# Kernel optimization log

Measured on AMD Instinct MI355X. Metric: run time of the kernel, lower is better.

## Reference

```python
import jax, jax.numpy as jnp
import numpy as np

N = 50000
E = 800000
IN_C = 128
HID = 256
OUT_C = 40


def setup_inputs() -> dict:
    key = jax.random.key(0)
    ks = jax.random.split(key, 12)
    def glorot(k, shape):
        lim = float(np.sqrt(6.0 / (shape[0] + shape[1])))
        return jax.random.uniform(k, shape, jnp.float32, -lim, lim)
    x = jax.random.normal(ks[0], (N, IN_C), jnp.float32)
    edge_index = jax.random.randint(ks[1], (2, E), 0, N, jnp.int64)
    edge_weight = jax.random.uniform(ks[2], (E,), jnp.float32)
    return {
        "x": x,
        "edge_index": edge_index,
        "edge_weight": edge_weight,
        "w1_rel": glorot(ks[3], (IN_C, HID)),
        "b1": jnp.zeros((HID,), jnp.float32),
        "w1_root": glorot(ks[4], (IN_C, HID)),
        "w2_rel": glorot(ks[5], (HID, HID)),
        "b2": jnp.zeros((HID,), jnp.float32),
        "w2_root": glorot(ks[6], (HID, HID)),
        "w_lin": glorot(ks[7], (2 * HID, OUT_C)),
        "b_lin": jnp.zeros((OUT_C,), jnp.float32),
    }


def graph_conv(x, src, dst, w, w_rel, b_rel, w_root):
    # PyG GraphConv (aggr='add'): lin_rel(scatter_add(x[src]*w)) + lin_root(x)
    msg = x[src] * w[:, None]                      # [E, F]
    agg = jax.ops.segment_sum(msg, dst, num_segments=N)  # [N, F]
    return agg @ w_rel + b_rel + x @ w_root


def reference(x, edge_index, edge_weight, w1_rel, b1, w1_root,
              w2_rel, b2, w2_root, w_lin, b_lin):
    src, dst = edge_index[0], edge_index[1]
    x1 = jax.nn.relu(graph_conv(x, src, dst, edge_weight, w1_rel, b1, w1_root))
    # dropout is a no-op in eval mode
    x2 = jax.nn.relu(graph_conv(x1, src, dst, edge_weight, w2_rel, b2, w2_root))
    h = jnp.concatenate([x1, x2], axis=-1)         # [N, 2*HID]
    logits = h @ w_lin + b_lin                     # [N, OUT_C]
    return jax.nn.log_softmax(logits, axis=-1)
```

## Files before the change

### kernel.cpp

```cpp
#include <hip/hip_runtime.h>
#include <hip/hip_bf16.h>
#include <hip/hip_fp16.h>
#include <math.h>


typedef __attribute__((ext_vector_type(8))) short short8;
typedef __attribute__((ext_vector_type(4))) float f32x4;

static __device__ __forceinline__ float bf2f(unsigned short u) {
    return __uint_as_float(((unsigned)u) << 16);
}

static __device__ __forceinline__ void fp8x4_to_f32(unsigned u, float* o) {
#if __has_builtin(__builtin_amdgcn_cvt_pk_f32_fp8)
    auto lo = __builtin_amdgcn_cvt_pk_f32_fp8((int)u, false);
    auto hi = __builtin_amdgcn_cvt_pk_f32_fp8((int)u, true);
    o[0] = lo[0]; o[1] = lo[1]; o[2] = hi[0]; o[3] = hi[1];
#else
#pragma unroll
    for (int i = 0; i < 4; ++i) {
        unsigned b = (u >> (8 * i)) & 0xffu;
        unsigned short hb = (unsigned short)(((b & 0x80u) << 8) | ((b & 0x7fu) << 7));
        o[i] = __half2float(__ushort_as_half(hb)) * 256.0f;
    }
#endif
}

static __device__ __forceinline__ unsigned f32_to_fp8(float f) {
    __half h = __float2half(f * 0.00390625f);
    unsigned short hb = __half_as_ushort(h);
    unsigned mag = hb & 0x7fffu;
    unsigned s = (hb >> 8) & 0x80u;
    unsigned v = (mag + 0x3fu + ((mag >> 7) & 1u)) >> 7;
    if (v > 0x7eu) v = 0x7eu;
    return s | v;
}

#define BH_EPB 16

__global__ __launch_bounds__(256) void prep_all(
    const int* __restrict__ ei, int E, int hist_blocks,
    int* __restrict__ bh_part,
    const float* __restrict__ x, __hip_bfloat16* __restrict__ xb,
    unsigned char* __restrict__ xb8, int NX8,
    const float* __restrict__ w1_rel, const float* __restrict__ w1_root,
    const float* __restrict__ w2_rel, const float* __restrict__ w2_root,
    const float* __restrict__ w_lin,
    __hip_bfloat16* __restrict__ w1relT, __hip_bfloat16* __restrict__ w1rootT,
    __hip_bfloat16* __restrict__ w2relT, __hip_bfloat16* __restrict__ w2rootT,
    __hip_bfloat16* __restrict__ wlinT)
{
    __shared__ int lh[256];
    const int t = threadIdx.x;
    if (blockIdx.x < (unsigned)hist_blocks) {
        lh[t] = 0;
        __syncthreads();
        const int base = blockIdx.x * (256 * BH_EPB);
#pragma unroll
        for (int i = 0; i < BH_EPB; ++i) {
            int e = base + i * 256 + t;
            if (e < E) atomicAdd(&lh[ei[E + e] >> 8], 1);
        }
        __syncthreads();
        bh_part[blockIdx.x * 256 + t] = lh[t];
        return;
    }
    int idx = (blockIdx.x - hist_blocks) * 256 + t;
    if (idx < NX8) {
        float4 a = *(const float4*)&x[(size_t)idx * 8];
        float4 b = *(const float4*)&x[(size_t)idx * 8 + 4];
        float f[8] = { a.x, a.y, a.z, a.w, b.x, b.y, b.z, b.w };
        __hip_bfloat16 o[8];
#pragma unroll
        for (int i = 0; i < 8; ++i) o[i] = __float2bfloat16(f[i]);
        *(short8*)&xb[(size_t)idx * 8] = *(short8*)o;
        unsigned p0 = 0, p1 = 0;
#pragma unroll
        for (int i = 0; i < 4; ++i) p0 |= f32_to_fp8(f[i]) << (8 * i);
#pragma unroll
        for (int i = 0; i < 4; ++i) p1 |= f32_to_fp8(f[4 + i]) << (8 * i);
        *(uint2*)&xb8[(size_t)idx * 8] = make_uint2(p0, p1);
        return;
    }
    idx -= NX8;
    if (idx < 65536) {
        const float* src = (idx < 32768) ? w1_rel : w1_root;
        __hip_bfloat16* dst = (idx < 32768) ? w1relT : w1rootT;
        int i = idx & 32767;
        int k = i >> 8, c = i & 255;
        dst[c * 128 + k] = __float2bfloat16(src[i]);
    } else if (idx < 196608) {
        int j = idx - 65536;
        const float* src = (j < 65536) ? w2_rel : w2_root;
        __hip_bfloat16* dst = (j < 65536) ? w2relT : w2rootT;
        int i = j & 65535;
        int k = i >> 8, c = i & 255;
        dst[c * 256 + k] = __float2bfloat16(src[i]);
    } else if (idx < 229376) {
        int i = idx - 196608;
        int seg = i >> 14, c = (i >> 8) & 63, k = i & 255;
        float v = (c < 40) ? w_lin[(size_t)(seg * 256 + k) * 40 + c] : 0.f;
        wlinT[i] = __float2bfloat16(v);
    }
}

__global__ __launch_bounds__(256) void scan_bsum(
    const int* __restrict__ bh_part, int hist_blocks,
    int* __restrict__ bpre, int* __restrict__ bend,
    int* __restrict__ bucket_cursor)
{
    __shared__ int sh[256];
    const int t = threadIdx.x;
    int a0 = 0, a1 = 0, a2 = 0, a3 = 0, a4 = 0, a5 = 0, a6 = 0, a7 = 0;
    int b = 0;
    for (; b + 8 <= hist_blocks; b += 8) {
        a0 += bh_part[(b + 0) * 256 + t];
        a1 += bh_part[(b + 1) * 256 + t];
        a2 += bh_part[(b + 2) * 256 + t];
        a3 += bh_part[(b + 3) * 256 + t];
        a4 += bh_part[(b + 4) * 256 + t];
        a5 += bh_part[(b + 5) * 256 + t];
        a6 += bh_part[(b + 6) * 256 + t];
        a7 += bh_part[(b + 7) * 256 + t];
    }
    for (; b < hist_blocks; ++b) a0 += bh_part[b * 256 + t];
    int v = ((a0 + a1) + (a2 + a3)) + ((a4 + a5) + (a6 + a7));
    sh[t] = v;
    __syncthreads();
#pragma unroll
    for (int off = 1; off < 256; off <<= 1) {
        int u = (t >= off) ? sh[t - off] : 0;
        __syncthreads();
        sh[t] += u;
        __syncthreads();
    }
    bpre[t]          = sh[t] - v;
    bend[t]          = sh[t];
    bucket_cursor[t] = sh[t] - v;
}

#define P1_EPB 8
__global__ __launch_bounds__(256) void part_kernel(
    const int* __restrict__ ei, const float* __restrict__ ew,
    int* __restrict__ bucket_cursor, uint2* __restrict__ part, int E)
{
    __shared__ int lhist[256];
    __shared__ int gbase[256];
    const int t = threadIdx.x;
    const int base = blockIdx.x * (256 * P1_EPB);
    lhist[t] = 0;
    __syncthreads();

    int pk[P1_EPB];
#pragma unroll
    for (int i = 0; i < P1_EPB; ++i) {
        int e = base + i * 256 + t;
        if (e < E) {
            int b = ei[E + e] >> 8;
            int r = atomicAdd(&lhist[b], 1);
            pk[i] = (b << 16) | r;
        } else pk[i] = -1;
    }
    __syncthreads();
    if (lhist[t] > 0) gbase[t] = atomicAdd(&bucket_cursor[t], lhist[t]);
    __syncthreads();
#pragma unroll
    for (int i = 0; i < P1_EPB; ++i) {
        if (pk[i] >= 0) {
            int e = base + i * 256 + t;
            int d = ei[E + e];
            unsigned short w16 = __half_as_ushort(__float2half(ew[e]));
            unsigned rec = ((unsigned)w16 << 16) | (unsigned)ei[e];
            int pos = gbase[pk[i] >> 16] + (pk[i] & 0xffff);
            part[pos] = make_uint2(rec, (unsigned)d);
        }
    }
}

__global__ __launch_bounds__(256) void fill2_kernel(
    const uint2* __restrict__ part, const int* __restrict__ bpre,
    const int* __restrict__ bend, int* __restrict__ row_ptr,
    unsigned* __restrict__ edges, int n)
{
    __shared__ int lcnt[256];
    __shared__ int excl[256];
    __shared__ int curs[256];
    const int b = blockIdx.x;
    const int t = threadIdx.x;
    const int node0 = b << 8;
    lcnt[t] = 0;
    __syncthreads();
    const int beg = bpre[b];
    const int end = bend[b];
    for (int i = beg + t; i < end; i += 256)
        atomicAdd(&lcnt[part[i].y & 255u], 1);
    __syncthreads();
    int v = lcnt[t];
    excl[t] = v;
    __syncthreads();
#pragma unroll
    for (int off = 1; off < 256; off <<= 1) {
        int u = (t >= off) ? excl[t - off] : 0;
        __syncthreads();
        excl[t] += u;
        __syncthreads();
    }
    const int base_t = beg + excl[t] - v;
    const int nd = node0 + t;
    if (nd <= n) row_ptr[nd] = base_t;
    curs[t] = base_t;
    __syncthreads();
    for (int i = beg + t; i < end; i += 256) {
        uint2 p = part[i];
        int slot = atomicAdd(&curs[p.y & 255u], 1);
        edges[slot] = p.x;
    }
}

template <int C>
__global__ __launch_bounds__(256) void gather_fp8(
    const unsigned char* __restrict__ feat8,
    const unsigned* __restrict__ edges,
    const int*  __restrict__ rp,
    __hip_bfloat16* __restrict__ agg, int n)
{
    const int node = (blockIdx.x * 256 + threadIdx.x) >> 6;
    const int lane = threadIdx.x & 63;
    if (node >= n) return;
    const int beg = __builtin_amdgcn_readfirstlane(rp[node]);
    const int end = __builtin_amdgcn_readfirstlane(rp[node + 1]);

    constexpr int EPW = (C == 128) ? 8 : 4;
    constexpr int LPR = 64 / EPW;
    const int es = lane / LPR;
    const int ch = lane % LPR;
    const unsigned coff = (unsigned)ch * 16;

    float acc[16] = {};

    auto accum16 = [&](uint4 u, float w) {
        unsigned uu[4] = { u.x, u.y, u.z, u.w };
#pragma unroll
        for (int q = 0; q < 4; ++q) {
            float f[4];
            fp8x4_to_f32(uu[q], f);
#pragma unroll
            for (int i = 0; i < 4; ++i)
                acc[q * 4 + i] = fmaf(f[i], w, acc[q * 4 + i]);
        }
    };

    auto unpack_w = [](unsigned p) {
        return __half2float(__ushort_as_half((unsigned short)(p >> 16)));
    };

    for (int base = beg; base < end; base += 64) {
        const int m = min(64, end - base);
        unsigned ev = edges[base + ((lane < m) ? lane : (m - 1))];
        if (lane >= m) ev &= 0xffffu;

        int s = 0;
        for (; s + 2 * EPW <= m; s += 2 * EPW) {
            int j0 = s + es, j1 = j0 + EPW;
            unsigned p0 = (unsigned)__shfl((int)ev, j0, 64);
            unsigned p1 = (unsigned)__shfl((int)ev, j1, 64);
            uint4 u0 = *(const uint4*)(feat8 + (size_t)(p0 & 0xffffu) * C + coff);
            uint4 u1 = *(const uint4*)(feat8 + (size_t)(p1 & 0xffffu) * C + coff);
            accum16(u0, unpack_w(p0));
            accum16(u1, unpack_w(p1));
        }
        for (; s < m; s += EPW) {
            int j = min(s + es, 63);
            unsigned p = (unsigned)__shfl((int)ev, j, 64);
            uint4 u = *(const uint4*)(feat8 + (size_t)(p & 0xffffu) * C + coff);
            accum16(u, unpack_w(p));
        }
    }

#pragma unroll
    for (int k = 0; k < 16; ++k) {
        if constexpr (C == 128) {
            acc[k] += __shfl_xor(acc[k], 8, 64);
            acc[k] += __shfl_xor(acc[k], 16, 64);
            acc[k] += __shfl_xor(acc[k], 32, 64);
        } else {
            acc[k] += __shfl_xor(acc[k], 16, 64);
            acc[k] += __shfl_xor(acc[k], 32, 64);
        }
    }
    if (es == 0) {
        __hip_bfloat16 o[16];
#pragma unroll
        for (int k = 0; k < 16; ++k) o[k] = __float2bfloat16(acc[k]);
        __hip_bfloat16* op = agg + (size_t)node * C + ch * 16;
        *(short8*)op       = *(short8*)o;
        *(short8*)(op + 8) = *(short8*)(o + 8);
    }
}

template <bool WRITE_FP8>
__global__ __launch_bounds__(256) void gemm_mfma(
    const __hip_bfloat16* __restrict__ A0, const __hip_bfloat16* __restrict__ A1,
    const __hip_bfloat16* __restrict__ W0T, const __hip_bfloat16* __restrict__ W1T,
    const float* __restrict__ bias,
    __hip_bfloat16* __restrict__ Cmat,
    unsigned char* __restrict__ Cfp8,
    int n, int K0, int K1)
{
    __shared__ __hip_bfloat16 Asl[2][128 * 64];
    __shared__ __hip_bfloat16 Bsl[2][128 * 64];
    const int bm = blockIdx.x >> 1;
    const int bn = blockIdx.x & 1;
    const int row0 = bm * 128, col0 = bn * 128;
    const int t = threadIdx.x, lane = t & 63, wid = t >> 6;
    const int wr = wid >> 1, wc = wid & 1;

    const int S0 = K0 >> 6;
    const int S  = S0 + (K1 >> 6);

    auto stage = [&](int buf, int s) {
        const __hip_bfloat16* A;
        const __hip_bfloat16* WT;
        int K, k0;
        if (s < S0) { A = A0; WT = W0T; K = K0; k0 = s << 6; }
        else        { A = A1; WT = W1T; K = K1; k0 = (s - S0) << 6; }
#pragma unroll
        for (int i = 0; i < 4; ++i) {
            int idx = i * 256 + t;
            int r = idx >> 3, c = idx & 7;
            int gr = row0 + r; if (gr >= n) gr = n - 1;
            const __hip_bfloat16* srcA =
                A + (size_t)gr * K + k0 + ((c ^ (r & 7)) << 3);
            __builtin_amdgcn_global_load_lds(
                (const __attribute__((address_space(1))) void*)srcA,
                (__attribute__((address_space(3))) void*)&Asl[buf][idx * 8], 16, 0, 0);
            const __hip_bfloat16* srcB =
                WT + (size_t)(col0 + r) * K + k0 + ((c ^ (r & 7)) << 3);
            __builtin_amdgcn_global_load_lds(
                (const __attribute__((address_space(1))) void*)srcB,
                (__attribute__((address_space(3))) void*)&Bsl[buf][idx * 8], 16, 0, 0);
        }
    };

    f32x4 acc[4][4] = {};

    stage(0, 0);
    __syncthreads();

    for (int s = 0; s < S; ++s) {
        const int buf = s & 1;
        if (s + 1 < S) stage(buf ^ 1, s + 1);
#pragma unroll
        for (int kh = 0; kh < 2; ++kh) {
            const int cchunk = kh * 4 + (lane >> 4);
            short8 af[4], bfr[4];
#pragma unroll
            for (int m = 0; m < 4; ++m) {
                int r = wr * 64 + m * 16 + (lane & 15);
                af[m] = *(const short8*)&Asl[buf][r * 64 + ((cchunk ^ (r & 7)) << 3)];
            }
#pragma unroll
            for (int nn = 0; nn < 4; ++nn) {
                int r = wc * 64 + nn * 16 + (lane & 15);
                bfr[nn] = *(const short8*)&Bsl[buf][r * 64 + ((cchunk ^ (r & 7)) << 3)];
            }
#pragma unroll
            for (int m = 0; m < 4; ++m)
#pragma unroll
                for (int nn = 0; nn < 4; ++nn)
                    acc[m][nn] = __builtin_amdgcn_mfma_f32_16x16x32_bf16(
                        af[m], bfr[nn], acc[m][nn], 0, 0, 0);
        }
        __syncthreads();
    }

    __hip_bfloat16* Csh = &Asl[0][0];
#pragma unroll
    for (int nn = 0; nn < 4; ++nn) {
        int lcol = wc * 64 + nn * 16 + (lane & 15);
        float b = bias[col0 + lcol];
#pragma unroll
        for (int m = 0; m < 4; ++m) {
#pragma unroll
            for (int rg = 0; rg < 4; ++rg) {
                int lrow = wr * 64 + m * 16 + ((lane >> 4) * 4) + rg;
                float v = fmaxf(acc[m][nn][rg] + b, 0.f);
                Csh[lrow * 128 + lcol] = __float2bfloat16(v);
            }
        }
    }
    __syncthreads();

#pragma unroll
    for (int it = 0; it < 8; ++it) {
        int idx = it * 256 + t;
        int r = idx >> 4, c16 = idx & 15;
        if (row0 + r < n)
            *(short8*)(Cmat + (size_t)(row0 + r) * 256 + col0 + c16 * 8) =
                *(const short8*)&Csh[r * 128 + c16 * 8];
    }
    if constexpr (WRITE_FP8) {
#pragma unroll
        for (int it = 0; it < 4; ++it) {
            int idx = it * 256 + t;
            int r = idx >> 3, c16 = idx & 7;
            if (row0 + r < n) {
                const __hip_bfloat16* src = &Csh[r * 128 + c16 * 16];
                unsigned w[4];
#pragma unroll
                for (int q = 0; q < 4; ++q) {
                    unsigned p = 0;
#pragma unroll
                    for (int i = 0; i < 4; ++i)
                        p |= f32_to_fp8(__bfloat162float(src[q * 4 + i])) << (8 * i);
                    w[q] = p;
                }
                *(uint4*)(Cfp8 + (size_t)(row0 + r) * 256 + col0 + c16 * 16) =
                    make_uint4(w[0], w[1], w[2], w[3]);
            }
        }
    }
}

__global__ __launch_bounds__(256) void head_mfma(
    const __hip_bfloat16* __restrict__ X1, const __hip_bfloat16* __restrict__ X2,
    const __hip_bfloat16* __restrict__ WLT,
    const float* __restrict__ b_lin,
    float* __restrict__ out, int n)
{
    __shared__ __hip_bfloat16 Asl[128 * 64];
    __shared__ __hip_bfloat16 Bsl[64 * 64];
    const int row0 = blockIdx.x * 128;
    const int t = threadIdx.x, lane = t & 63, wid = t >> 6;

    f32x4 acc[2][4] = {};

    for (int seg = 0; seg < 2; ++seg) {
        const __hip_bfloat16* A  = seg ? X2 : X1;
        const __hip_bfloat16* WT = WLT + seg * 64 * 256;
        for (int k0 = 0; k0 < 256; k0 += 64) {
#pragma unroll
            for (int i = 0; i < 4; ++i) {
                int idx = i * 256 + t;
                int r = idx >> 3, c = idx & 7;
                int gr = row0 + r; if (gr >= n) gr = n - 1;
                const __hip_bfloat16* srcA =
                    A + (size_t)gr * 256 + k0 + ((c ^ (r & 7)) << 3);
                __builtin_amdgcn_global_load_lds(
                    (const __attribute__((address_space(1))) void*)srcA,
                    (__attribute__((address_space(3))) void*)&Asl[idx * 8], 16, 0, 0);
            }
#pragma unroll
            for (int i = 0; i < 2; ++i) {
                int idx = i * 256 + t;
                int r = idx >> 3, c = idx & 7;
                const __hip_bfloat16* srcB =
                    WT + (size_t)r * 256 + k0 + ((c ^ (r & 7)) << 3);
                __builtin_amdgcn_global_load_lds(
                    (const __attribute__((address_space(1))) void*)srcB,
                    (__attribute__((address_space(3))) void*)&Bsl[idx * 8], 16, 0, 0);
            }
            __syncthreads();
#pragma unroll
            for (int kh = 0; kh < 2; ++kh) {
                const int cchunk = kh * 4 + (lane >> 4);
                short8 af[2], bfr[4];
#pragma unroll
                for (int m = 0; m < 2; ++m) {
                    int r = wid * 32 + m * 16 + (lane & 15);
                    af[m] = *(const short8*)&Asl[r * 64 + ((cchunk ^ (r & 7)) << 3)];
                }
#pragma unroll
                for (int nn = 0; nn < 4; ++nn) {
                    int r = nn * 16 + (lane & 15);
                    bfr[nn] = *(const short8*)&Bsl[r * 64 + ((cchunk ^ (r & 7)) << 3)];
                }
#pragma unroll
                for (int m = 0; m < 2; ++m)
#pragma unroll
                    for (int nn = 0; nn < 4; ++nn)
                        acc[m][nn] = __builtin_amdgcn_mfma_f32_16x16x32_bf16(
                            af[m], bfr[nn], acc[m][nn], 0, 0, 0);
            }
            __syncthreads();
        }
    }

    const int cl = lane & 15;
    float bb[4];
#pragma unroll
    for (int nn = 0; nn < 4; ++nn) {
        int col = nn * 16 + cl;
        bb[nn] = (col < 40) ? b_lin[col] : 0.f;
    }
#pragma unroll
    for (int m = 0; m < 2; ++m) {
#pragma unroll
        for (int rg = 0; rg < 4; ++rg) {
            float v[4];
            float mx = -1e30f;
#pragma unroll
            for (int nn = 0; nn < 4; ++nn) {
                int col = nn * 16 + cl;
                v[nn] = acc[m][nn][rg] + bb[nn];
                if (col < 40) mx = fmaxf(mx, v[nn]);
            }
#pragma unroll
            for (int off = 1; off < 16; off <<= 1)
                mx = fmaxf(mx, __shfl_xor(mx, off, 64));
            float s = 0.f;
#pragma unroll
            for (int nn = 0; nn < 4; ++nn) {
                int col = nn * 16 + cl;
                if (col < 40) s += expf(v[nn] - mx);
            }
#pragma unroll
            for (int off = 1; off < 16; off <<= 1)
                s += __shfl_xor(s, off, 64);
            float ls = logf(s);
            int row = row0 + wid * 32 + m * 16 + ((lane >> 4) * 4) + rg;
            if (row < n) {
#pragma unroll
                for (int nn = 0; nn < 4; ++nn) {
                    int col = nn * 16 + cl;
                    if (col < 40)
                        out[(size_t)row * 40 + col] = v[nn] - mx - ls;
                }
            }
        }
    }
}

extern "C" void kernel_launch(void* const* d_in, const int* in_sizes, int n_in,
                              void* d_out, int out_size, void* d_ws, size_t ws_size,
                              hipStream_t stream)
{
    const float* x       = (const float*)d_in[0];
    const int*   ei      = (const int*)  d_in[1];
    const float* ew      = (const float*)d_in[2];
    const float* w1_rel  = (const float*)d_in[3];
    const float* b1      = (const float*)d_in[4];
    const float* w1_root = (const float*)d_in[5];
    const float* w2_rel  = (const float*)d_in[6];
    const float* b2      = (const float*)d_in[7];
    const float* w2_root = (const float*)d_in[8];
    const float* w_lin   = (const float*)d_in[9];
    const float* b_lin   = (const float*)d_in[10];
    float* out = (float*)d_out;

    const int N = in_sizes[0] / 128;
    const int E = in_sizes[2];

    auto align = [](char*& p, size_t bytes) {
        char* r = p;
        p += (bytes + 255) & ~(size_t)255;
        return r;
    };
    char* wp = (char*)d_ws;
    __hip_bfloat16* xb     = (__hip_bfloat16*)align(wp, (size_t)N * 128 * 2);
    __hip_bfloat16* agg1b  = (__hip_bfloat16*)align(wp, (size_t)N * 128 * 2);
    __hip_bfloat16* x1b    = (__hip_bfloat16*)align(wp, (size_t)N * 256 * 2);
    __hip_bfloat16* agg2b  = (__hip_bfloat16*)align(wp, (size_t)N * 256 * 2);
    __hip_bfloat16* x2b    = (__hip_bfloat16*)align(wp, (size_t)N * 256 * 2);
    unsigned char*  xb8    = (unsigned char*)align(wp, (size_t)N * 128);
    unsigned char*  x1b8   = (unsigned char*)align(wp, (size_t)N * 256);
    __hip_bfloat16* w1relT  = (__hip_bfloat16*)align(wp, 256 * 128 * 2);
    __hip_bfloat16* w1rootT = (__hip_bfloat16*)align(wp, 256 * 128 * 2);
    __hip_bfloat16* w2relT  = (__hip_bfloat16*)align(wp, 256 * 256 * 2);
    __hip_bfloat16* w2rootT = (__hip_bfloat16*)align(wp, 256 * 256 * 2);
    __hip_bfloat16* wlinT   = (__hip_bfloat16*)align(wp, 2 * 64 * 256 * 2);
    int*      row_ptr       = (int*)align(wp, (size_t)(N + 1) * 4);
    int*      bh_part       = (int*)align(wp, 256 * 256 * 4);
    int*      bpre          = (int*)align(wp, 256 * 4);
    int*      bend          = (int*)align(wp, 256 * 4);
    int*      bucket_cursor = (int*)align(wp, 256 * 4);
    unsigned* edges         = (unsigned*)align(wp, (size_t)E * 4);
    uint2*    part          = (uint2*)align(wp, (size_t)E * 8);

    const int nb = (N + 255) / 256;
    const int hist_blocks = (E + 256 * BH_EPB - 1) / (256 * BH_EPB);
    const int NX8 = N * 128 / 8;

    {
        long long conv = (long long)NX8 + 229376;
        int conv_blocks = (int)((conv + 255) / 256);
        prep_all<<<hist_blocks + conv_blocks, 256, 0, stream>>>(
            ei, E, hist_blocks, bh_part,
            x, xb, xb8, NX8,
            w1_rel, w1_root, w2_rel, w2_root, w_lin,
            w1relT, w1rootT, w2relT, w2rootT, wlinT);
    }
    {
        scan_bsum<<<1, 256, 0, stream>>>(bh_part, hist_blocks,
                                         bpre, bend, bucket_cursor);
        int p1_blocks = (E + 256 * P1_EPB - 1) / (256 * P1_EPB);
        part_kernel<<<p1_blocks, 256, 0, stream>>>(ei, ew, bucket_cursor, part, E);
        fill2_kernel<<<nb, 256, 0, stream>>>(part, bpre, bend, row_ptr, edges, N);
    }

    const int gather_blocks = (N * 64 + 255) / 256;
    const int gemm_grid     = ((N + 127) / 128) * 2;
    const int head_grid     = (N + 127) / 128;

    gather_fp8<128><<<gather_blocks, 256, 0, stream>>>(
        xb8, edges, row_ptr, agg1b, N);
    gemm_mfma<true><<<gemm_grid, 256, 0, stream>>>(
        agg1b, xb, w1relT, w1rootT, b1, x1b, x1b8, N, 128, 128);
    gather_fp8<256><<<gather_blocks, 256, 0, stream>>>(
        x1b8, edges, row_ptr, agg2b, N);
    gemm_mfma<false><<<gemm_grid, 256, 0, stream>>>(
        agg2b, x1b, w2relT, w2rootT, b2, x2b, nullptr, N, 256, 256);
    head_mfma<<<head_grid, 256, 0, stream>>>(x1b, x2b, wlinT, b_lin, out, N);
}
```

Measured before the change: 179.9 us.

## Shrink GEMM and head tiles to raise occupancy and double-buffer head

The GEMM kernel moves from 128x128 output tiles with a K-step of 64 to 128x64 tiles with a K-step of 32, which cuts LDS use and doubles the grid so more blocks fit per CU. The head kernel drops from 128-row to 64-row tiles and gains a double-buffered LDS pipeline, so loads for the next step overlap MFMA work instead of stalling on a sync. In exchange, A-tile data is reused less per block and more barriers run per unit of work in the GEMM.

```diff
diff --git a/kernel.cpp b/kernel.cpp
--- a/kernel.cpp
+++ b/kernel.cpp
@@ -307,42 +307,45 @@
     unsigned char* __restrict__ Cfp8,
     int n, int K0, int K1)
 {
-    __shared__ __hip_bfloat16 Asl[2][128 * 64];
-    __shared__ __hip_bfloat16 Bsl[2][128 * 64];
-    const int bm = blockIdx.x >> 1;
-    const int bn = blockIdx.x & 1;
-    const int row0 = bm * 128, col0 = bn * 128;
+    __shared__ __hip_bfloat16 smem[12288];
+    const int bm = blockIdx.x >> 2;
+    const int bn = blockIdx.x & 3;
+    const int row0 = bm * 128, col0 = bn * 64;
     const int t = threadIdx.x, lane = t & 63, wid = t >> 6;
-    const int wr = wid >> 1, wc = wid & 1;
-
-    const int S0 = K0 >> 6;
-    const int S  = S0 + (K1 >> 6);
+
+    const int S0 = K0 >> 5;
+    const int S  = S0 + (K1 >> 5);
 
     auto stage = [&](int buf, int s) {
         const __hip_bfloat16* A;
         const __hip_bfloat16* WT;
         int K, k0;
-        if (s < S0) { A = A0; WT = W0T; K = K0; k0 = s << 6; }
-        else        { A = A1; WT = W1T; K = K1; k0 = (s - S0) << 6; }
-#pragma unroll
-        for (int i = 0; i < 4; ++i) {
+        if (s < S0) { A = A0; WT = W0T; K = K0; k0 = s << 5; }
+        else        { A = A1; WT = W1T; K = K1; k0 = (s - S0) << 5; }
+        __hip_bfloat16* Ab = smem + buf * 4096;
+        __hip_bfloat16* Bb = smem + 8192 + buf * 2048;
+#pragma unroll
+        for (int i = 0; i < 2; ++i) {
             int idx = i * 256 + t;
-            int r = idx >> 3, c = idx & 7;
+            int r = idx >> 2, c = idx & 3;
             int gr = row0 + r; if (gr >= n) gr = n - 1;
             const __hip_bfloat16* srcA =
-                A + (size_t)gr * K + k0 + ((c ^ (r & 7)) << 3);
+                A + (size_t)gr * K + k0 + ((c ^ (r & 3)) << 3);
             __builtin_amdgcn_global_load_lds(
                 (const __attribute__((address_space(1))) void*)srcA,
-                (__attribute__((address_space(3))) void*)&Asl[buf][idx * 8], 16, 0, 0);
+                (__attribute__((address_space(3))) void*)&Ab[idx * 8], 16, 0, 0);
+        }
+        {
+            int r = t >> 2, c = t & 3;
             const __hip_bfloat16* srcB =
-                WT + (size_t)(col0 + r) * K + k0 + ((c ^ (r & 7)) << 3);
+                WT + (size_t)(col0 + r) * K + k0 + ((c ^ (r & 3)) << 3);
             __builtin_amdgcn_global_load_lds(
                 (const __attribute__((address_space(1))) void*)srcB,
-                (__attribute__((address_space(3))) void*)&Bsl[buf][idx * 8], 16, 0, 0);
+                (__attribute__((address_space(3))) void*)&Bb[t * 8], 16, 0, 0);
         }
     };
 
-    f32x4 acc[4][4] = {};
+    f32x4 acc[2][4] = {};
 
     stage(0, 0);
     __syncthreads();
@@ -350,62 +353,61 @@
     for (int s = 0; s < S; ++s) {
         const int buf = s & 1;
         if (s + 1 < S) stage(buf ^ 1, s + 1);
-#pragma unroll
-        for (int kh = 0; kh < 2; ++kh) {
-            const int cchunk = kh * 4 + (lane >> 4);
-            short8 af[4], bfr[4];
-#pragma unroll
-            for (int m = 0; m < 4; ++m) {
-                int r = wr * 64 + m * 16 + (lane & 15);
-                af[m] = *(const short8*)&Asl[buf][r * 64 + ((cchunk ^ (r & 7)) << 3)];
+        const __hip_bfloat16* Ab = smem + buf * 4096;
+        const __hip_bfloat16* Bb = smem + 8192 + buf * 2048;
+        const int cchunk = lane >> 4;
+        short8 af[2], bfr[4];
+#pragma unroll
+        for (int m = 0; m < 2; ++m) {
+            int r = wid * 32 + m * 16 + (lane & 15);
+            af[m] = *(const short8*)&Ab[r * 32 + ((cchunk ^ (r & 3)) << 3)];
+        }
+#pragma unroll
+        for (int nn = 0; nn < 4; ++nn) {
+            int r = nn * 16 + (lane & 15);
+            bfr[nn] = *(const short8*)&Bb[r * 32 + ((cchunk ^ (r & 3)) << 3)];
+        }
+#pragma unroll
+        for (int m = 0; m < 2; ++m)
+#pragma unroll
+            for (int nn = 0; nn < 4; ++nn)
+                acc[m][nn] = __builtin_amdgcn_mfma_f32_16x16x32_bf16(
+                    af[m], bfr[nn], acc[m][nn], 0, 0, 0);
+        __syncthreads();
+    }
+
+    __hip_bfloat16* Csh = smem;
+#pragma unroll
+    for (int nn = 0; nn < 4; ++nn) {
+        int lcol = nn * 16 + (lane & 15);
+        float b = bias[col0 + lcol];
+#pragma unroll
+        for (int m = 0; m < 2; ++m) {
+#pragma unroll
+            for (int rg = 0; rg < 4; ++rg) {
+                int lrow = wid * 32 + m * 16 + ((lane >> 4) * 4) + rg;
+                float v = fmaxf(acc[m][nn][rg] + b, 0.f);
+                Csh[lrow * 64 + lcol] = __float2bfloat16(v);
             }
-#pragma unroll
-            for (int nn = 0; nn < 4; ++nn) {
-                int r = wc * 64 + nn * 16 + (lane & 15);
-                bfr[nn] = *(const short8*)&Bsl[buf][r * 64 + ((cchunk ^ (r & 7)) << 3)];
-            }
-#pragma unroll
-            for (int m = 0; m < 4; ++m)
-#pragma unroll
-                for (int nn = 0; nn < 4; ++nn)
-                    acc[m][nn] = __builtin_amdgcn_mfma_f32_16x16x32_bf16(
-                        af[m], bfr[nn], acc[m][nn], 0, 0, 0);
-        }
-        __syncthreads();
-    }
-
-    __hip_bfloat16* Csh = &Asl[0][0];
-#pragma unroll
-    for (int nn = 0; nn < 4; ++nn) {
-        int lcol = wc * 64 + nn * 16 + (lane & 15);
-        float b = bias[col0 + lcol];
-#pragma unroll
-        for (int m = 0; m < 4; ++m) {
-#pragma unroll
-            for (int rg = 0; rg < 4; ++rg) {
-                int lrow = wr * 64 + m * 16 + ((lane >> 4) * 4) + rg;
-                float v = fmaxf(acc[m][nn][rg] + b, 0.f);
-                Csh[lrow * 128 + lcol] = __float2bfloat16(v);
-            }
-        }
-    }
-    __syncthreads();
-
-#pragma unroll
-    for (int it = 0; it < 8; ++it) {
+        }
+    }
+    __syncthreads();
+
+#pragma unroll
+    for (int it = 0; it < 4; ++it) {
         int idx = it * 256 + t;
-        int r = idx >> 4, c16 = idx & 15;
+        int r = idx >> 3, c8 = idx & 7;
         if (row0 + r < n)
-            *(short8*)(Cmat + (size_t)(row0 + r) * 256 + col0 + c16 * 8) =
-                *(const short8*)&Csh[r * 128 + c16 * 8];
+            *(short8*)(Cmat + (size_t)(row0 + r) * 256 + col0 + c8 * 8) =
+                *(const short8*)&Csh[r * 64 + c8 * 8];
     }
     if constexpr (WRITE_FP8) {
 #pragma unroll
-        for (int it = 0; it < 4; ++it) {
+        for (int it = 0; it < 2; ++it) {
             int idx = it * 256 + t;
-            int r = idx >> 3, c16 = idx & 7;
+            int r = idx >> 2, c16 = idx & 3;
             if (row0 + r < n) {
-                const __hip_bfloat16* src = &Csh[r * 128 + c16 * 16];
+                const __hip_bfloat16* src = &Csh[r * 64 + c16 * 16];
                 unsigned w[4];
 #pragma unroll
                 for (int q = 0; q < 4; ++q) {
@@ -428,62 +430,67 @@
     const float* __restrict__ b_lin,
     float* __restrict__ out, int n)
 {
-    __shared__ __hip_bfloat16 Asl[128 * 64];
-    __shared__ __hip_bfloat16 Bsl[64 * 64];
-    const int row0 = blockIdx.x * 128;
+    __shared__ __hip_bfloat16 smem[16384];
+    const int row0 = blockIdx.x * 64;
     const int t = threadIdx.x, lane = t & 63, wid = t >> 6;
 
-    f32x4 acc[2][4] = {};
-
-    for (int seg = 0; seg < 2; ++seg) {
+    auto stage = [&](int buf, int s) {
+        const int seg = s >> 2;
+        const int k0  = (s & 3) << 6;
         const __hip_bfloat16* A  = seg ? X2 : X1;
         const __hip_bfloat16* WT = WLT + seg * 64 * 256;
-        for (int k0 = 0; k0 < 256; k0 += 64) {
-#pragma unroll
-            for (int i = 0; i < 4; ++i) {
-                int idx = i * 256 + t;
-                int r = idx >> 3, c = idx & 7;
-                int gr = row0 + r; if (gr >= n) gr = n - 1;
-                const __hip_bfloat16* srcA =
-                    A + (size_t)gr * 256 + k0 + ((c ^ (r & 7)) << 3);
-                __builtin_amdgcn_global_load_lds(
-                    (const __attribute__((address_space(1))) void*)srcA,
-                    (__attribute__((address_space(3))) void*)&Asl[idx * 8], 16, 0, 0);
+        __hip_bfloat16* Ab = smem + buf * 4096;
+        __hip_bfloat16* Bb = smem + 8192 + buf * 4096;
+#pragma unroll
+        for (int i = 0; i < 2; ++i) {
+            int idx = i * 256 + t;
+            int r = idx >> 3, c = idx & 7;
+            int gr = row0 + r; if (gr >= n) gr = n - 1;
+            const __hip_bfloat16* srcA =
+                A + (size_t)gr * 256 + k0 + ((c ^ (r & 7)) << 3);
+            __builtin_amdgcn_global_load_lds(
+                (const __attribute__((address_space(1))) void*)srcA,
+                (__attribute__((address_space(3))) void*)&Ab[idx * 8], 16, 0, 0);
+        }
+#pragma unroll
+        for (int i = 0; i < 2; ++i) {
+            int idx = i * 256 + t;
+            int r = idx >> 3, c = idx & 7;
+            const __hip_bfloat16* srcB =
+                WT + (size_t)r * 256 + k0 + ((c ^ (r & 7)) << 3);
+            __builtin_amdgcn_global_load_lds(
+                (const __attribute__((address_space(1))) void*)srcB,
+                (__attribute__((address_space(3))) void*)&Bb[idx * 8], 16, 0, 0);
+        }
+    };
+
+    f32x4 acc[4] = {};
+
+    stage(0, 0);
+    __syncthreads();
+
+    for (int s = 0; s < 8; ++s) {
+        const int buf = s & 1;
+        if (s + 1 < 8) stage(buf ^ 1, s + 1);
+        const __hip_bfloat16* Ab = smem + buf * 4096;
+        const __hip_bfloat16* Bb = smem + 8192 + buf * 4096;
+#pragma unroll
+        for (int kh = 0; kh < 2; ++kh) {
+            const int cchunk = kh * 4 + (lane >> 4);
+            int ra = wid * 16 + (lane & 15);
+            short8 af = *(const short8*)&Ab[ra * 64 + ((cchunk ^ (ra & 7)) << 3)];
+            short8 bfr[4];
+#pragma unroll
+            for (int nn = 0; nn < 4; ++nn) {
+                int r = nn * 16 + (lane & 15);
+                bfr[nn] = *(const short8*)&Bb[r * 64 + ((cchunk ^ (r & 7)) << 3)];
             }
 #pragma unroll
-            for (int i = 0; i < 2; ++i) {
-                int idx = i * 256 + t;
-                int r = idx >> 3, c = idx & 7;
-                const __hip_bfloat16* srcB =
-                    WT + (size_t)r * 256 + k0 + ((c ^ (r & 7)) << 3);
-                __builtin_amdgcn_global_load_lds(
-                    (const __attribute__((address_space(1))) void*)srcB,
-                    (__attribute__((address_space(3))) void*)&Bsl[idx * 8], 16, 0, 0);
-            }
-            __syncthreads();
-#pragma unroll
-            for (int kh = 0; kh < 2; ++kh) {
-                const int cchunk = kh * 4 + (lane >> 4);
-                short8 af[2], bfr[4];
-#pragma unroll
-                for (int m = 0; m < 2; ++m) {
-                    int r = wid * 32 + m * 16 + (lane & 15);
-                    af[m] = *(const short8*)&Asl[r * 64 + ((cchunk ^ (r & 7)) << 3)];
-                }
-#pragma unroll
-                for (int nn = 0; nn < 4; ++nn) {
-                    int r = nn * 16 + (lane & 15);
-                    bfr[nn] = *(const short8*)&Bsl[r * 64 + ((cchunk ^ (r & 7)) << 3)];
-                }
-#pragma unroll
-                for (int m = 0; m < 2; ++m)
-#pragma unroll
-                    for (int nn = 0; nn < 4; ++nn)
-                        acc[m][nn] = __builtin_amdgcn_mfma_f32_16x16x32_bf16(
-                            af[m], bfr[nn], acc[m][nn], 0, 0, 0);
-            }
-            __syncthreads();
-        }
+            for (int nn = 0; nn < 4; ++nn)
+                acc[nn] = __builtin_amdgcn_mfma_f32_16x16x32_bf16(
+                    af, bfr[nn], acc[nn], 0, 0, 0);
+        }
+        __syncthreads();
     }
 
     const int cl = lane & 15;
@@ -494,38 +501,35 @@
         bb[nn] = (col < 40) ? b_lin[col] : 0.f;
     }
 #pragma unroll
-    for (int m = 0; m < 2; ++m) {
-#pragma unroll
-        for (int rg = 0; rg < 4; ++rg) {
-            float v[4];
-            float mx = -1e30f;
+    for (int rg = 0; rg < 4; ++rg) {
+        float v[4];
+        float mx = -1e30f;
+#pragma unroll
+        for (int nn = 0; nn < 4; ++nn) {
+            int col = nn * 16 + cl;
+            v[nn] = acc[nn][rg] + bb[nn];
+            if (col < 40) mx = fmaxf(mx, v[nn]);
+        }
+#pragma unroll
+        for (int off = 1; off < 16; off <<= 1)
+            mx = fmaxf(mx, __shfl_xor(mx, off, 64));
+        float s = 0.f;
+#pragma unroll
+        for (int nn = 0; nn < 4; ++nn) {
+            int col = nn * 16 + cl;
+            if (col < 40) s += expf(v[nn] - mx);
+        }
+#pragma unroll
+        for (int off = 1; off < 16; off <<= 1)
+            s += __shfl_xor(s, off, 64);
+        float ls = logf(s);
+        int row = row0 + wid * 16 + ((lane >> 4) * 4) + rg;
+        if (row < n) {
 #pragma unroll
             for (int nn = 0; nn < 4; ++nn) {
                 int col = nn * 16 + cl;
-                v[nn] = acc[m][nn][rg] + bb[nn];
-                if (col < 40) mx = fmaxf(mx, v[nn]);
-            }
-#pragma unroll
-            for (int off = 1; off < 16; off <<= 1)
-                mx = fmaxf(mx, __shfl_xor(mx, off, 64));
-            float s = 0.f;
-#pragma unroll
-            for (int nn = 0; nn < 4; ++nn) {
-                int col = nn * 16 + cl;
-                if (col < 40) s += expf(v[nn] - mx);
-            }
-#pragma unroll
-            for (int off = 1; off < 16; off <<= 1)
-                s += __shfl_xor(s, off, 64);
-            float ls = logf(s);
-            int row = row0 + wid * 32 + m * 16 + ((lane >> 4) * 4) + rg;
-            if (row < n) {
-#pragma unroll
-                for (int nn = 0; nn < 4; ++nn) {
-                    int col = nn * 16 + cl;
-                    if (col < 40)
-                        out[(size_t)row * 40 + col] = v[nn] - mx - ls;
-                }
+                if (col < 40)
+                    out[(size_t)row * 40 + col] = v[nn] - mx - ls;
             }
         }
     }
@@ -599,8 +603,8 @@
     }
 
     const int gather_blocks = (N * 64 + 255) / 256;
-    const int gemm_grid     = ((N + 127) / 128) * 2;
-    const int head_grid     = (N + 127) / 128;
+    const int gemm_grid     = ((N + 127) / 128) * 4;
+    const int head_grid     = (N + 63) / 64;
 
     gather_fp8<128><<<gather_blocks, 256, 0, stream>>>(
         xb8, edges, row_ptr, agg1b, N);
```

Result: slower. 189.5 us (+5.3%).
